# Kernel optimization log

Hardware: AMD Instinct MI355X
Metric: run time of the kernel (lower is better)

The kernel has to match this reference:

```python
import jax, jax.numpy as jnp
import numpy as np

N, E, ND, ED, H, L = 50000, 800000, 64, 32, 128, 4
MIN = 2 * H + H + 1  # message MLP input dim = 385
EPS = 1e-5


def _layernorm(x, w, b):
    mu = x.mean(-1, keepdims=True)
    var = ((x - mu) ** 2).mean(-1, keepdims=True)
    return (x - mu) / jnp.sqrt(var + EPS) * w + b


def setup_inputs() -> dict:
    key = jax.random.key(0)
    ks = jax.random.split(key, 40)

    def w(k, shape):
        return jax.random.normal(k, shape, jnp.float32) / np.sqrt(shape[-2]).astype(np.float32)

    inp = {
        "node_features": jax.random.normal(ks[0], (N, ND), jnp.float32),
        "edge_features": jax.random.normal(ks[1], (E, ED), jnp.float32),
        "congestion": jax.random.uniform(ks[2], (N,), jnp.float32),
        "edge_index": jax.random.randint(ks[3], (2, E), 0, N),
        "unrouted_mask": jax.random.randint(ks[4], (N,), 0, 2).astype(jnp.bool_),
        "enc_node_w": w(ks[5], (ND, H)), "enc_node_b": jnp.zeros(H),
        "enc_edge_w": w(ks[6], (ED, H)), "enc_edge_b": jnp.zeros(H),
        "msg_w1": w(ks[7], (L, MIN, H)), "msg_b1": jnp.zeros((L, H)),
        "msg_w2": w(ks[8], (L, H, H)), "msg_b2": jnp.zeros((L, H)),
        "upd_w1": w(ks[9], (L, 2 * H, H)), "upd_b1": jnp.zeros((L, H)),
        "upd_w2": w(ks[10], (L, H, H)), "upd_b2": jnp.zeros((L, H)),
        "ln_w": jnp.ones((L, H)), "ln_b": jnp.zeros((L, H)),
        "unr_w1": w(ks[11], (1, H)), "unr_b1": jnp.zeros(H),
        "unr_w2": w(ks[12], (H, H)), "unr_b2": jnp.zeros(H),
        "ro_w1": w(ks[13], (2 * H, H)), "ro_b1": jnp.zeros(H),
        "ro_w2": w(ks[14], (H, H // 2)), "ro_b2": jnp.zeros(H // 2),
        "ro_w3": w(ks[15], (H // 2, 1)), "ro_b3": jnp.zeros(1),
    }
    return inp


def reference(node_features, edge_features, congestion, edge_index, unrouted_mask,
              enc_node_w, enc_node_b, enc_edge_w, enc_edge_b,
              msg_w1, msg_b1, msg_w2, msg_b2,
              upd_w1, upd_b1, upd_w2, upd_b2,
              ln_w, ln_b,
              unr_w1, unr_b1, unr_w2, unr_b2,
              ro_w1, ro_b1, ro_w2, ro_b2, ro_w3, ro_b3):
    n = node_features.shape[0]
    src, dst = edge_index[0], edge_index[1]

    x = node_features @ enc_node_w + enc_node_b            # [N, H]
    ea = edge_features @ enc_edge_w + enc_edge_b           # [E, H]
    cong_src = congestion[src][:, None]                    # [E, 1]

    for l in range(msg_w1.shape[0]):
        # message: gather src/dst features, concat with edge attr + congestion
        m_in = jnp.concatenate([x[src], x[dst], ea, cong_src], axis=-1)  # [E, 385]
        m = jax.nn.relu(m_in @ msg_w1[l] + msg_b1[l]) @ msg_w2[l] + msg_b2[l]  # [E, H]
        agg = jax.ops.segment_sum(m, dst, num_segments=n)  # scatter_add over dst
        u_in = jnp.concatenate([x, agg], axis=-1)          # [N, 2H]
        x_new = jax.nn.relu(u_in @ upd_w1[l] + upd_b1[l]) @ upd_w2[l] + upd_b2[l]
        x = _layernorm(x + x_new, ln_w[l], ln_b[l])        # dropout = identity (eval)

    graph_embed = x.mean(axis=0, keepdims=True)            # [1, H] (batch=None branch)
    unrouted_frac = unrouted_mask.astype(jnp.float32).mean()[None, None]  # [1, 1]
    unr = jax.nn.relu(unrouted_frac @ unr_w1 + unr_b1) @ unr_w2 + unr_b2  # [1, H]
    combined = jnp.concatenate([graph_embed, unr], axis=-1)  # [1, 2H]
    h = jax.nn.relu(combined @ ro_w1 + ro_b1)
    h = jax.nn.relu(h @ ro_w2 + ro_b2)
    out = jax.nn.sigmoid(h @ ro_w3 + ro_b3)                # [1, 1]
    return out.squeeze(-1)                                 # [1]
```

## Files before the change

### kernel.cpp

```cpp
#include <hip/hip_runtime.h>
#include <hip/hip_fp16.h>
#include <math.h>

#define NN 50000
#define EE 800000

typedef _Float16 half8 __attribute__((ext_vector_type(8)));
typedef float floatx4 __attribute__((ext_vector_type(4)));

__global__ void fold_kernel(const float* __restrict__ ew, const float* __restrict__ eb,
                            const float* __restrict__ w1, const float* __restrict__ b1,
                            float* __restrict__ Wc, float* __restrict__ b1f) {
  int l = blockIdx.y, c = blockIdx.x, j = threadIdx.x;
  __shared__ float row[128];
  const float* w1l = w1 + (size_t)l * 385 * 128;
  if (c < 32) {
    row[j] = ew[c * 128 + j];
    __syncthreads();
    float acc = 0.f;
    for (int k = 0; k < 128; k++) acc += row[k] * w1l[(256 + k) * 128 + j];
    Wc[((size_t)l * 32 + c) * 128 + j] = acc;
  } else {
    row[j] = eb[j];
    __syncthreads();
    float acc = b1[l * 128 + j];
    for (int k = 0; k < 128; k++) acc += row[k] * w1l[(256 + k) * 128 + j];
    b1f[l * 128 + j] = acc;
  }
}

__global__ void prep_w(const float* __restrict__ src, _Float16* __restrict__ dst,
                       int K, int perm) {
  int l = blockIdx.y;
  int lane = threadIdx.x;
  int kc = blockIdx.x >> 3, nt = blockIdx.x & 7;
  int n = nt * 16 + (lane & 15);
  int k0 = kc * 32 + (lane >> 4) * 8;
  const float* s = src + (size_t)l * K * 128;
  _Float16 out[8];
  for (int j = 0; j < 8; j++) {
    int k = k0 + j;
    int ks = perm ? ((k & 7) * 16 + (k >> 3)) : k;
    out[j] = (_Float16)s[(size_t)ks * 128 + n];
  }
  _Float16* d = dst + (((size_t)l * gridDim.x + blockIdx.x) * 64 + lane) * 8;
  *(half8*)d = *(half8*)out;
}

__global__ void prep_cong(const float* __restrict__ mw1, _Float16* __restrict__ w1cp) {
  int l = blockIdx.x, p = threadIdx.x;
  int col = (p & 7) * 16 + (p >> 3);
  w1cp[l * 128 + p] = (_Float16)mw1[((size_t)l * 385 + 384) * 128 + col];
}

__global__ void hist_kernel(const int* __restrict__ dstv, int* __restrict__ counts) {
  int e = blockIdx.x * 256 + threadIdx.x;
  if (e < EE) atomicAdd(&counts[dstv[e]], 1);
}

__global__ void scan_kernel(const int* __restrict__ counts, int* __restrict__ offs) {
  __shared__ int ws[16];
  int t = threadIdx.x, lane = t & 63, w = t >> 6;
  int carry = 0;
  for (int chunk = 0; chunk < 49; chunk++) {
    int i = chunk * 1024 + t;
    int v = (i < NN) ? counts[i] : 0;
    int s = v;
    for (int off = 1; off < 64; off <<= 1) {
      int u = __shfl_up(s, off);
      if (lane >= off) s += u;
    }
    if (lane == 63) ws[w] = s;
    __syncthreads();
    if (w == 0) {
      int u = (lane < 16) ? ws[lane] : 0;
      for (int off = 1; off < 16; off <<= 1) {
        int x = __shfl_up(u, off);
        if (lane >= off && lane < 16) u += x;
      }
      if (lane < 16) ws[lane] = u;
    }
    __syncthreads();
    int wbase = (w > 0) ? ws[w - 1] : 0;
    int total = ws[15];
    if (i < NN) offs[i] = carry + wbase + s - v;
    carry += total;
    __syncthreads();
  }
}

__global__ void slot_kernel(const int* __restrict__ srcv, const int* __restrict__ dstv,
                            const float* __restrict__ cong, const float* __restrict__ ef,
                            const int* __restrict__ offs, int* __restrict__ cursor,
                            int* __restrict__ srcp, int* __restrict__ dstp,
                            float* __restrict__ cgp, _Float16* __restrict__ efh) {
  int e = blockIdx.x * 256 + threadIdx.x;
  if (e >= EE) return;
  int d = dstv[e], s = srcv[e];
  int p = offs[d] + atomicAdd(&cursor[d], 1);
  srcp[p] = s;
  dstp[p] = d;
  cgp[p] = cong[s];
  const float* sp = ef + (size_t)e * 32;
  _Float16* dp = efh + (size_t)p * 32;
  for (int i = 0; i < 4; i++) {
    float4 f = *(const float4*)(sp + i * 8);
    float4 g = *(const float4*)(sp + i * 8 + 4);
    half8 v;
    v[0] = (_Float16)f.x; v[1] = (_Float16)f.y; v[2] = (_Float16)f.z; v[3] = (_Float16)f.w;
    v[4] = (_Float16)g.x; v[5] = (_Float16)g.y; v[6] = (_Float16)g.z; v[7] = (_Float16)g.w;
    *(half8*)(dp + i * 8) = v;
  }
}

__global__ void enc_mfma(const float* __restrict__ nf, const _Float16* __restrict__ Wenc,
                         const float* __restrict__ bn, _Float16* __restrict__ xh) {
  int t = threadIdx.x, wave = t >> 6, lane = t & 63;
  int quad = lane >> 4, l15 = lane & 15;
  long nb0 = (long)blockIdx.x * 64 + wave * 16;
  long rn = nb0 + l15;
  if (rn >= NN) rn = NN - 1;

  floatx4 acc[8] = {};
  for (int kc = 0; kc < 2; kc++) {
    const float* p = nf + rn * 64 + kc * 32 + quad * 8;
    float4 f0 = *(const float4*)p;
    float4 f1 = *(const float4*)(p + 4);
    half8 a;
    a[0] = (_Float16)f0.x; a[1] = (_Float16)f0.y;
    a[2] = (_Float16)f0.z; a[3] = (_Float16)f0.w;
    a[4] = (_Float16)f1.x; a[5] = (_Float16)f1.y;
    a[6] = (_Float16)f1.z; a[7] = (_Float16)f1.w;
    const _Float16* bp = Wenc + (size_t)(kc * 8) * 512 + lane * 8;
    for (int nt = 0; nt < 8; nt++) {
      half8 b = *(const half8*)(bp + nt * 512);
      acc[nt] = __builtin_amdgcn_mfma_f32_16x16x32_f16(a, b, acc[nt], 0, 0, 0);
    }
  }
  float bv[8];
  for (int nt = 0; nt < 8; nt++) bv[nt] = bn[nt * 16 + l15];
  for (int reg = 0; reg < 4; reg++) {
    long n = nb0 + quad * 4 + reg;
    if (n < NN) {
      for (int nt = 0; nt < 8; nt++)
        xh[n * 128 + nt * 16 + l15] = (_Float16)(acc[nt][reg] + bv[nt]);
    }
  }
}

__global__ __launch_bounds__(256, 3) void sd_kernel(
    const _Float16* __restrict__ xh, const _Float16* __restrict__ WSa,
    const _Float16* __restrict__ WSb, const float* __restrict__ b1f,
    _Float16* __restrict__ Sh, _Float16* __restrict__ Dh) {
  int t = threadIdx.x, wave = t >> 6, lane = t & 63;
  int quad = lane >> 4, l15 = lane & 15;
  long nb0 = (long)blockIdx.x * 64 + wave * 16;
  long rn = nb0 + l15;
  if (rn >= NN) rn = NN - 1;

  floatx4 as_[8] = {}, ad[8] = {};
#pragma unroll
  for (int kc = 0; kc < 4; kc++) {
    half8 a = *(const half8*)(xh + rn * 128 + kc * 32 + quad * 8);
    const _Float16* bpa = WSa + (size_t)(kc * 8) * 512 + lane * 8;
    const _Float16* bpb = WSb + (size_t)(kc * 8) * 512 + lane * 8;
#pragma unroll
    for (int nt = 0; nt < 8; nt++) {
      half8 ba = *(const half8*)(bpa + nt * 512);
      half8 bb = *(const half8*)(bpb + nt * 512);
      as_[nt] = __builtin_amdgcn_mfma_f32_16x16x32_f16(a, ba, as_[nt], 0, 0, 0);
      ad[nt] = __builtin_amdgcn_mfma_f32_16x16x32_f16(a, bb, ad[nt], 0, 0, 0);
    }
  }
  float bbv[8];
  for (int nt = 0; nt < 8; nt++) bbv[nt] = b1f[nt * 16 + l15];
  for (int reg = 0; reg < 4; reg++) {
    long n = nb0 + quad * 4 + reg;
    if (n < NN) {
      half8 hs, hd;
      for (int nt = 0; nt < 8; nt++) {
        hs[nt] = (_Float16)as_[nt][reg];
        hd[nt] = (_Float16)(ad[nt][reg] + bbv[nt]);
      }
      *(half8*)(Sh + n * 128 + l15 * 8) = hs;
      *(half8*)(Dh + n * 128 + l15 * 8) = hd;
    }
  }
}

__global__ __launch_bounds__(256, 4) void msg_kernel(
    const _Float16* __restrict__ Sh, const _Float16* __restrict__ Dh,
    const _Float16* __restrict__ efh, const float* __restrict__ cgp,
    const int* __restrict__ srcp, const int* __restrict__ dstp,
    const _Float16* __restrict__ Wcp, const _Float16* __restrict__ Wp2,
    const _Float16* __restrict__ w1cp, const float* __restrict__ b2,
    __half* __restrict__ agg) {
  __shared__ __align__(16) _Float16 As[128][136];
  __shared__ int s_src[128], s_dst[128];
  __shared__ float s_cg[128];
  int t = threadIdx.x, wave = t >> 6, lane = t & 63;
  int quad = lane >> 4, l15 = lane & 15;
  long eb0 = (long)blockIdx.x * 128;
  int web = wave * 32;
  if (t < 128) {
    s_src[t] = srcp[eb0 + t];
    s_dst[t] = dstp[eb0 + t];
    s_cg[t] = cgp[eb0 + t];
  }
  __syncthreads();

  half8 wcl = *(const half8*)(w1cp + l15 * 8);

#pragma unroll
  for (int mtl = 0; mtl < 2; mtl++) {
    int rbase = web + mtl * 16;
    half8 sv[4], dv[4];
#pragma unroll
    for (int reg = 0; reg < 4; reg++) {
      int r = rbase + quad * 4 + reg;
      sv[reg] = *(const half8*)(Sh + (size_t)s_src[r] * 128 + l15 * 8);
      dv[reg] = *(const half8*)(Dh + (size_t)s_dst[r] * 128 + l15 * 8);
    }
    half8 a = *(const half8*)(efh + (size_t)(eb0 + rbase + l15) * 32 + quad * 8);
    floatx4 e[8] = {};
#pragma unroll
    for (int nt = 0; nt < 8; nt++) {
      half8 b = *(const half8*)(Wcp + (size_t)nt * 512 + lane * 8);
      e[nt] = __builtin_amdgcn_mfma_f32_16x16x32_f16(a, b, e[nt], 0, 0, 0);
    }
#pragma unroll
    for (int reg = 0; reg < 4; reg++) {
      int r = rbase + quad * 4 + reg;
      float cg = s_cg[r];
      half8 hv;
#pragma unroll
      for (int nt = 0; nt < 8; nt++) {
        float v = (float)sv[reg][nt] + (float)dv[reg][nt] + e[nt][reg] +
                  cg * (float)wcl[nt];
        hv[nt] = (_Float16)fmaxf(v, 0.f);
      }
      *(half8*)&As[r][l15 * 8] = hv;
    }
  }
  __syncthreads();

  int nb = wave * 2;
  floatx4 acc2[8][2] = {};
#pragma unroll
  for (int kc = 0; kc < 4; kc++) {
    const _Float16* bp = Wp2 + ((size_t)(kc * 8 + nb)) * 512 + lane * 8;
    half8 b0 = *(const half8*)bp;
    half8 b1v = *(const half8*)(bp + 512);
#pragma unroll
    for (int mt = 0; mt < 8; mt++) {
      half8 a = *(const half8*)&As[mt * 16 + l15][kc * 32 + quad * 8];
      acc2[mt][0] = __builtin_amdgcn_mfma_f32_16x16x32_f16(a, b0, acc2[mt][0], 0, 0, 0);
      acc2[mt][1] = __builtin_amdgcn_mfma_f32_16x16x32_f16(a, b1v, acc2[mt][1], 0, 0, 0);
    }
  }
  __syncthreads();

  {
    float c0 = b2[nb * 16 + l15], c1 = b2[(nb + 1) * 16 + l15];
#pragma unroll
    for (int mt = 0; mt < 8; mt++)
#pragma unroll
      for (int reg = 0; reg < 4; reg++) {
        int row = mt * 16 + quad * 4 + reg;
#pragma unroll
        for (int ntp = 0; ntp < 2; ntp++) {
          float v = acc2[mt][ntp][reg] + (ntp ? c1 : c0);
          float p = __shfl_xor(v, 1);
          if ((l15 & 1) == 0) {
            __half2 h = __halves2half2(__float2half(v), __float2half(p));
            *(__half2*)&As[row][(nb + ntp) * 16 + l15] = h;
          }
        }
      }
  }
  __syncthreads();

  {
    int cp = t & 63;
    int q = t >> 6;
    int r0 = q * 32;
    __half2 vals[32];
#pragma unroll
    for (int i = 0; i < 32; i++) vals[i] = *(__half2*)&As[r0 + i][cp * 2];
    int cur = s_dst[r0];
    float a0 = 0.f, a1 = 0.f;
    for (int i = 0; i < 32; i++) {
      int d = s_dst[r0 + i];
      if (d != cur) {
        unsafeAtomicAdd((__half2*)(agg + (long)cur * 128 + cp * 2),
                        __halves2half2(__float2half(a0), __float2half(a1)));
        a0 = a1 = 0.f;
        cur = d;
      }
      float2 f = __half22float2(vals[i]);
      a0 += f.x;
      a1 += f.y;
    }
    unsafeAtomicAdd((__half2*)(agg + (long)cur * 128 + cp * 2),
                    __halves2half2(__float2half(a0), __float2half(a1)));
  }
}

__global__ __launch_bounds__(256, 3) void upd_kernel(
    _Float16* __restrict__ xh, const _Float16* __restrict__ agg,
    const _Float16* __restrict__ Wp1, const _Float16* __restrict__ Wp2,
    const float* __restrict__ b1, const float* __restrict__ b2,
    const float* __restrict__ g, const float* __restrict__ bb) {
  __shared__ __align__(16) _Float16 hs[4][16][136];
  int t = threadIdx.x, wave = t >> 6, lane = t & 63;
  int quad = lane >> 4, l15 = lane & 15;
  long nb0 = (long)blockIdx.x * 64 + wave * 16;

  floatx4 acc[8] = {};
  {
    long n = nb0 + l15;
    long rn = n < NN ? n : NN - 1;
    for (int kc = 0; kc < 8; kc++) {
      half8 a;
      if (kc < 4) {
        a = *(const half8*)(xh + rn * 128 + kc * 32 + quad * 8);
      } else {
        a = *(const half8*)(agg + rn * 128 + (kc - 4) * 32 + quad * 8);
      }
      const _Float16* bp = Wp1 + (size_t)(kc * 8) * 512 + lane * 8;
      for (int nt = 0; nt < 8; nt++) {
        half8 b = *(const half8*)(bp + nt * 512);
        acc[nt] = __builtin_amdgcn_mfma_f32_16x16x32_f16(a, b, acc[nt], 0, 0, 0);
      }
    }
  }

  float bbv[8];
  for (int nt = 0; nt < 8; nt++) bbv[nt] = b1[nt * 16 + l15];
  for (int reg = 0; reg < 4; reg++) {
    half8 hv;
    for (int nt = 0; nt < 8; nt++)
      hv[nt] = (_Float16)fmaxf(acc[nt][reg] + bbv[nt], 0.f);
    *(half8*)&hs[wave][quad * 4 + reg][l15 * 8] = hv;
  }
  __syncthreads();

  floatx4 acc2[8] = {};
  for (int kc = 0; kc < 4; kc++) {
    half8 a = *(const half8*)&hs[wave][l15][kc * 32 + quad * 8];
    const _Float16* bp = Wp2 + (size_t)(kc * 8) * 512 + lane * 8;
    for (int nt = 0; nt < 8; nt++) {
      half8 b = *(const half8*)(bp + nt * 512);
      acc2[nt] = __builtin_amdgcn_mfma_f32_16x16x32_f16(a, b, acc2[nt], 0, 0, 0);
    }
  }

  float b2v[8], gv[8], bv[8];
  for (int nt = 0; nt < 8; nt++) {
    int col = nt * 16 + l15;
    b2v[nt] = b2[col]; gv[nt] = g[col]; bv[nt] = bb[col];
  }
  for (int reg = 0; reg < 4; reg++) {
    long n = nb0 + quad * 4 + reg;
    bool ok = n < NN;
    long rn = ok ? n : NN - 1;
    float y[8];
    float s = 0.f;
    for (int nt = 0; nt < 8; nt++) {
      y[nt] = (float)xh[rn * 128 + nt * 16 + l15] + acc2[nt][reg] + b2v[nt];
      s += y[nt];
    }
    s += __shfl_xor(s, 1); s += __shfl_xor(s, 2);
    s += __shfl_xor(s, 4); s += __shfl_xor(s, 8);
    float mu = s * (1.f / 128.f);
    float q = 0.f;
    for (int nt = 0; nt < 8; nt++) {
      y[nt] -= mu;
      q += y[nt] * y[nt];
    }
    q += __shfl_xor(q, 1); q += __shfl_xor(q, 2);
    q += __shfl_xor(q, 4); q += __shfl_xor(q, 8);
    float rstd = rsqrtf(q * (1.f / 128.f) + 1e-5f);
    if (ok) {
      for (int nt = 0; nt < 8; nt++) {
        float o = y[nt] * rstd * gv[nt] + bv[nt];
        xh[n * 128 + nt * 16 + l15] = (_Float16)o;
      }
    }
  }
}

__global__ void reduce_kernel(const _Float16* __restrict__ xh,
                              const int* __restrict__ umask, float* __restrict__ red) {
  int t = threadIdx.x;
  long base = (long)blockIdx.x * 196;
  int j = t & 127, half = t >> 7;
  float acc = 0.f;
  for (int i = 0; i < 98; i++) {
    long n = base + half + 2L * i;
    if (n < NN) acc += (float)xh[n * 128 + j];
  }
  __shared__ float sr[2][128];
  __shared__ float sm[4];
  sr[half][j] = acc;
  float mv = 0.f;
  {
    long n = base + t;
    if (t < 196 && n < NN) mv = (float)umask[n];
  }
  for (int off = 32; off; off >>= 1) mv += __shfl_xor(mv, off);
  if ((t & 63) == 0) sm[t >> 6] = mv;
  __syncthreads();
  if (t < 128) atomicAdd(&red[t], sr[0][t] + sr[1][t]);
  if (t == 0) atomicAdd(&red[128], sm[0] + sm[1] + sm[2] + sm[3]);
}

__global__ void readout_kernel(const float* __restrict__ red,
                               const float* __restrict__ xw1, const float* __restrict__ xb1,
                               const float* __restrict__ xw2, const float* __restrict__ xb2,
                               const float* __restrict__ rw1, const float* __restrict__ rb1,
                               const float* __restrict__ rw2, const float* __restrict__ rb2,
                               const float* __restrict__ rw3, const float* __restrict__ rb3,
                               float* __restrict__ out) {
  __shared__ float sa[128], sb[128], sc[128];
  int j = threadIdx.x;
  const float inv = 1.f / (float)NN;
  float ge = red[j] * inv;
  float uf = red[128] * inv;
  float u1 = fmaxf(uf * xw1[j] + xb1[j], 0.f);
  sa[j] = u1;
  sb[j] = ge;
  __syncthreads();
  float u2 = xb2[j];
  for (int k = 0; k < 128; k++) u2 += sa[k] * xw2[k * 128 + j];
  sc[j] = u2;
  __syncthreads();
  float h1 = rb1[j];
  for (int k = 0; k < 128; k++) h1 += sb[k] * rw1[k * 128 + j];
  for (int k = 0; k < 128; k++) h1 += sc[k] * rw1[(128 + k) * 128 + j];
  h1 = fmaxf(h1, 0.f);
  __syncthreads();
  sa[j] = h1;
  __syncthreads();
  float h2 = 0.f;
  if (j < 64) {
    h2 = rb2[j];
    for (int k = 0; k < 128; k++) h2 += sa[k] * rw2[k * 64 + j];
    h2 = fmaxf(h2, 0.f);
  }
  __syncthreads();
  if (j < 64) sb[j] = h2;
  __syncthreads();
  if (j == 0) {
    float a = rb3[0];
    for (int k = 0; k < 64; k++) a += sb[k] * rw3[k];
    out[0] = 1.f / (1.f + expf(-a));
  }
}

extern "C" void kernel_launch(void* const* d_in, const int* in_sizes, int n_in,
                              void* d_out, int out_size, void* d_ws, size_t ws_size,
                              hipStream_t stream) {
  const float* nf   = (const float*)d_in[0];
  const float* ef   = (const float*)d_in[1];
  const float* cong = (const float*)d_in[2];
  const int*   eidx = (const int*)d_in[3];
  const int*   um   = (const int*)d_in[4];
  const float* enw  = (const float*)d_in[5];
  const float* enb  = (const float*)d_in[6];
  const float* eew  = (const float*)d_in[7];
  const float* eeb  = (const float*)d_in[8];
  const float* mw1  = (const float*)d_in[9];
  const float* mb1  = (const float*)d_in[10];
  const float* mw2  = (const float*)d_in[11];
  const float* mb2  = (const float*)d_in[12];
  const float* uw1  = (const float*)d_in[13];
  const float* ub1  = (const float*)d_in[14];
  const float* uw2  = (const float*)d_in[15];
  const float* ub2  = (const float*)d_in[16];
  const float* lnw  = (const float*)d_in[17];
  const float* lnb  = (const float*)d_in[18];
  const float* xw1  = (const float*)d_in[19];
  const float* xb1  = (const float*)d_in[20];
  const float* xw2  = (const float*)d_in[21];
  const float* xb2  = (const float*)d_in[22];
  const float* rw1  = (const float*)d_in[23];
  const float* rb1  = (const float*)d_in[24];
  const float* rw2  = (const float*)d_in[25];
  const float* rb2  = (const float*)d_in[26];
  const float* rw3  = (const float*)d_in[27];
  const float* rb3  = (const float*)d_in[28];
  float* out = (float*)d_out;

  char* W = (char*)d_ws;
  _Float16* xh    = (_Float16*)(W + 0);
  __half*   agg   = (__half*)(W + 12800000);
  _Float16* efh   = (_Float16*)(W + 25600000);
  _Float16* Sh    = (_Float16*)(W + 76800000);
  _Float16* Dh    = (_Float16*)(W + 89600000);
  int*      srcp  = (int*)(W + 102400000);
  int*      dstp  = (int*)(W + 105600000);
  float*    cgp   = (float*)(W + 108800000);
  int*      counts= (int*)(W + 112000000);
  int*      cursor= (int*)(W + 112200000);
  int*      offs  = (int*)(W + 112400000);
  _Float16* WSa   = (_Float16*)(W + 112600000);
  _Float16* WSb   = (_Float16*)(W + 112731072);
  _Float16* Wcp   = (_Float16*)(W + 112862144);
  _Float16* Wm2   = (_Float16*)(W + 112894912);
  _Float16* Wu1   = (_Float16*)(W + 113025984);
  _Float16* Wu2   = (_Float16*)(W + 113288128);
  _Float16* Wen   = (_Float16*)(W + 113419200);
  float*    Wc    = (float*)(W + 113435584);
  float*    b1f   = (float*)(W + 113501120);
  _Float16* w1cp  = (_Float16*)(W + 113503168);
  float*    red   = (float*)(W + 113504192);

  const int* srcv = eidx;
  const int* dstv = eidx + EE;

  (void)hipMemsetAsync(counts, 0, 400000, stream);
  hist_kernel<<<3125, 256, 0, stream>>>(dstv, counts);
  scan_kernel<<<1, 1024, 0, stream>>>(counts, offs);
  slot_kernel<<<3125, 256, 0, stream>>>(srcv, dstv, cong, ef, offs, cursor,
                                        srcp, dstp, cgp, efh);

  fold_kernel<<<dim3(33, 4), 128, 0, stream>>>(eew, eeb, mw1, mb1, Wc, b1f);
  prep_w<<<dim3(8, 4), 64, 0, stream>>>(Wc, Wcp, 32, 0);
  prep_w<<<dim3(32, 4), 64, 0, stream>>>(mw1, WSa, 385, 0);
  prep_w<<<dim3(32, 4), 64, 0, stream>>>(mw1 + 128 * 128, WSb, 385, 0);
  prep_w<<<dim3(32, 4), 64, 0, stream>>>(mw2, Wm2, 128, 1);
  prep_w<<<dim3(64, 4), 64, 0, stream>>>(uw1, Wu1, 256, 0);
  prep_w<<<dim3(32, 4), 64, 0, stream>>>(uw2, Wu2, 128, 1);
  prep_w<<<dim3(16, 1), 64, 0, stream>>>(enw, Wen, 64, 0);
  prep_cong<<<4, 128, 0, stream>>>(mw1, w1cp);
  enc_mfma<<<782, 256, 0, stream>>>(nf, Wen, enb, xh);

  for (int l = 0; l < 4; l++) {
    sd_kernel<<<782, 256, 0, stream>>>(
        xh, WSa + (size_t)l * 32 * 512, WSb + (size_t)l * 32 * 512,
        b1f + l * 128, Sh, Dh);
    (void)hipMemsetAsync(agg, 0, (size_t)NN * 128 * sizeof(__half), stream);
    msg_kernel<<<6250, 256, 0, stream>>>(
        Sh, Dh, efh, cgp, srcp, dstp,
        Wcp + (size_t)l * 8 * 512, Wm2 + (size_t)l * 32 * 512,
        w1cp + l * 128, mb2 + l * 128, agg);
    upd_kernel<<<782, 256, 0, stream>>>(
        xh, (const _Float16*)agg,
        Wu1 + (size_t)l * 64 * 512, Wu2 + (size_t)l * 32 * 512,
        ub1 + l * 128, ub2 + l * 128, lnw + l * 128, lnb + l * 128);
  }

  (void)hipMemsetAsync(red, 0, 129 * sizeof(float), stream);
  reduce_kernel<<<256, 256, 0, stream>>>(xh, um, red);
  readout_kernel<<<1, 128, 0, stream>>>(red, xw1, xb1, xw2, xb2,
                                        rw1, rb1, rw2, rb2, rw3, rb3, out);
}
```

Baseline: 958.1 us.

## Parallelize CSR offset scan and split edge sorting into inverse-permutation passes

Replaces the single-block serial prefix scan over node counts with a two-level multi-block scan. The edge slotting is split into one pass that computes an inverse permutation with atomics and a second pass that gathers per sorted slot, so writes become coalesced. Source and destination indices are packed into one int2 array, and congestion is now gathered on the fly in the message kernel instead of being pre-permuted. This adds extra kernel launches and a random congestion gather per layer in exchange for cheaper preprocessing.

After: 931.5 us. 2.8% less time.

```diff
diff --git a/kernel.cpp b/kernel.cpp
--- a/kernel.cpp
+++ b/kernel.cpp
@@ -58,49 +58,64 @@
   if (e < EE) atomicAdd(&counts[dstv[e]], 1);
 }
 
-__global__ void scan_kernel(const int* __restrict__ counts, int* __restrict__ offs) {
+__global__ void scan1_kernel(const int* __restrict__ counts, int* __restrict__ offs,
+                             int* __restrict__ bsum) {
   __shared__ int ws[16];
   int t = threadIdx.x, lane = t & 63, w = t >> 6;
-  int carry = 0;
-  for (int chunk = 0; chunk < 49; chunk++) {
-    int i = chunk * 1024 + t;
-    int v = (i < NN) ? counts[i] : 0;
-    int s = v;
-    for (int off = 1; off < 64; off <<= 1) {
-      int u = __shfl_up(s, off);
-      if (lane >= off) s += u;
-    }
-    if (lane == 63) ws[w] = s;
-    __syncthreads();
-    if (w == 0) {
-      int u = (lane < 16) ? ws[lane] : 0;
-      for (int off = 1; off < 16; off <<= 1) {
-        int x = __shfl_up(u, off);
-        if (lane >= off && lane < 16) u += x;
-      }
-      if (lane < 16) ws[lane] = u;
-    }
-    __syncthreads();
-    int wbase = (w > 0) ? ws[w - 1] : 0;
-    int total = ws[15];
-    if (i < NN) offs[i] = carry + wbase + s - v;
-    carry += total;
-    __syncthreads();
-  }
-}
-
-__global__ void slot_kernel(const int* __restrict__ srcv, const int* __restrict__ dstv,
-                            const float* __restrict__ cong, const float* __restrict__ ef,
-                            const int* __restrict__ offs, int* __restrict__ cursor,
-                            int* __restrict__ srcp, int* __restrict__ dstp,
-                            float* __restrict__ cgp, _Float16* __restrict__ efh) {
+  int i = blockIdx.x * 1024 + t;
+  int v = (i < NN) ? counts[i] : 0;
+  int s = v;
+  for (int off = 1; off < 64; off <<= 1) {
+    int u = __shfl_up(s, off);
+    if (lane >= off) s += u;
+  }
+  if (lane == 63) ws[w] = s;
+  __syncthreads();
+  if (w == 0) {
+    int u = (lane < 16) ? ws[lane] : 0;
+    for (int off = 1; off < 16; off <<= 1) {
+      int x = __shfl_up(u, off);
+      if (lane >= off && lane < 16) u += x;
+    }
+    if (lane < 16) ws[lane] = u;
+  }
+  __syncthreads();
+  int wbase = (w > 0) ? ws[w - 1] : 0;
+  if (i < NN) offs[i] = wbase + s - v;
+  if (t == 0) bsum[blockIdx.x] = ws[15];
+}
+
+__global__ void scan2_kernel(int* __restrict__ bsum) {
+  int t = threadIdx.x;
+  int v = (t < 49) ? bsum[t] : 0;
+  int s = v;
+  for (int off = 1; off < 64; off <<= 1) {
+    int u = __shfl_up(s, off);
+    if (t >= off) s += u;
+  }
+  if (t < 49) bsum[t] = s - v;
+}
+
+__global__ void slot1_kernel(const int* __restrict__ dstv, const int* __restrict__ offs,
+                             const int* __restrict__ bsum, int* __restrict__ cursor,
+                             int* __restrict__ einv) {
   int e = blockIdx.x * 256 + threadIdx.x;
   if (e >= EE) return;
-  int d = dstv[e], s = srcv[e];
-  int p = offs[d] + atomicAdd(&cursor[d], 1);
-  srcp[p] = s;
-  dstp[p] = d;
-  cgp[p] = cong[s];
+  int d = dstv[e];
+  int p = offs[d] + bsum[d >> 10] + atomicAdd(&cursor[d], 1);
+  einv[p] = e;
+}
+
+__global__ void slot2_kernel(const int* __restrict__ einv, const int* __restrict__ srcv,
+                             const int* __restrict__ dstv, const float* __restrict__ ef,
+                             int2* __restrict__ meta, _Float16* __restrict__ efh) {
+  int p = blockIdx.x * 256 + threadIdx.x;
+  if (p >= EE) return;
+  int e = einv[p];
+  int2 m;
+  m.x = srcv[e];
+  m.y = dstv[e];
+  meta[p] = m;
   const float* sp = ef + (size_t)e * 32;
   _Float16* dp = efh + (size_t)p * 32;
   for (int i = 0; i < 4; i++) {
@@ -190,8 +205,8 @@
 
 __global__ __launch_bounds__(256, 4) void msg_kernel(
     const _Float16* __restrict__ Sh, const _Float16* __restrict__ Dh,
-    const _Float16* __restrict__ efh, const float* __restrict__ cgp,
-    const int* __restrict__ srcp, const int* __restrict__ dstp,
+    const _Float16* __restrict__ efh, const int2* __restrict__ meta,
+    const float* __restrict__ cong,
     const _Float16* __restrict__ Wcp, const _Float16* __restrict__ Wp2,
     const _Float16* __restrict__ w1cp, const float* __restrict__ b2,
     __half* __restrict__ agg) {
@@ -203,9 +218,10 @@
   long eb0 = (long)blockIdx.x * 128;
   int web = wave * 32;
   if (t < 128) {
-    s_src[t] = srcp[eb0 + t];
-    s_dst[t] = dstp[eb0 + t];
-    s_cg[t] = cgp[eb0 + t];
+    int2 m = meta[eb0 + t];
+    s_src[t] = m.x;
+    s_dst[t] = m.y;
+    s_cg[t] = cong[m.x];
   }
   __syncthreads();
 
@@ -498,9 +514,8 @@
   _Float16* efh   = (_Float16*)(W + 25600000);
   _Float16* Sh    = (_Float16*)(W + 76800000);
   _Float16* Dh    = (_Float16*)(W + 89600000);
-  int*      srcp  = (int*)(W + 102400000);
-  int*      dstp  = (int*)(W + 105600000);
-  float*    cgp   = (float*)(W + 108800000);
+  int2*     meta  = (int2*)(W + 102400000);
+  int*      einv  = (int*)(W + 108800000);
   int*      counts= (int*)(W + 112000000);
   int*      cursor= (int*)(W + 112200000);
   int*      offs  = (int*)(W + 112400000);
@@ -515,15 +530,17 @@
   float*    b1f   = (float*)(W + 113501120);
   _Float16* w1cp  = (_Float16*)(W + 113503168);
   float*    red   = (float*)(W + 113504192);
+  int*      bsum  = (int*)red;
 
   const int* srcv = eidx;
   const int* dstv = eidx + EE;
 
   (void)hipMemsetAsync(counts, 0, 400000, stream);
   hist_kernel<<<3125, 256, 0, stream>>>(dstv, counts);
-  scan_kernel<<<1, 1024, 0, stream>>>(counts, offs);
-  slot_kernel<<<3125, 256, 0, stream>>>(srcv, dstv, cong, ef, offs, cursor,
-                                        srcp, dstp, cgp, efh);
+  scan1_kernel<<<49, 1024, 0, stream>>>(counts, offs, bsum);
+  scan2_kernel<<<1, 64, 0, stream>>>(bsum);
+  slot1_kernel<<<3125, 256, 0, stream>>>(dstv, offs, bsum, cursor, einv);
+  slot2_kernel<<<3125, 256, 0, stream>>>(einv, srcv, dstv, ef, meta, efh);
 
   fold_kernel<<<dim3(33, 4), 128, 0, stream>>>(eew, eeb, mw1, mb1, Wc, b1f);
   prep_w<<<dim3(8, 4), 64, 0, stream>>>(Wc, Wcp, 32, 0);
@@ -542,7 +559,7 @@
         b1f + l * 128, Sh, Dh);
     (void)hipMemsetAsync(agg, 0, (size_t)NN * 128 * sizeof(__half), stream);
     msg_kernel<<<6250, 256, 0, stream>>>(
-        Sh, Dh, efh, cgp, srcp, dstp,
+        Sh, Dh, efh, meta, cong,
         Wcp + (size_t)l * 8 * 512, Wm2 + (size_t)l * 32 * 512,
         w1cp + l * 128, mb2 + l * 128, agg);
     upd_kernel<<<782, 256, 0, stream>>>(
```
